# Kernel optimization log

Measured on AMD Instinct MI355X. Metric: run time of the kernel, lower is better.

## Reference

```python
import jax, jax.numpy as jnp
import numpy as np

N_NODES = 50000
N_EDGES = 800000
D = 64


def setup_inputs() -> dict:
    key = jax.random.key(0)
    k1, k2, k3, k4, k5 = jax.random.split(key, 5)
    x = jax.random.normal(k1, (N_NODES, D), dtype=jnp.float32)
    edge_index = jax.random.randint(k2, (2, N_EDGES), 0, N_NODES, dtype=jnp.int64)
    edge_weight = jax.random.uniform(k3, (N_EDGES,), dtype=jnp.float32)
    W = jax.random.normal(k4, (D, D), dtype=jnp.float32) / np.sqrt(D)
    b = jax.random.normal(k5, (D,), dtype=jnp.float32) * 0.01
    return {"x": x, "edge_index": edge_index, "edge_weight": edge_weight, "W": W, "b": b}


def reference(x, edge_index, edge_weight, W, b):
    # GCNConv (PyG defaults): add self-loops (weight 1), symmetric normalization,
    # linear transform then normalized scatter-add aggregation, bias, then ReLU.
    n = x.shape[0]
    loop = jnp.arange(n, dtype=edge_index.dtype)
    src = jnp.concatenate([edge_index[0], loop])          # [E+N] message sources
    dst = jnp.concatenate([edge_index[1], loop])          # [E+N] message targets
    ew = jnp.concatenate([edge_weight, jnp.ones((n,), dtype=x.dtype)])
    # degree on target nodes from edge weights
    deg = jax.ops.segment_sum(ew, dst, num_segments=n)
    dinv = jnp.where(deg > 0, jax.lax.rsqrt(deg), 0.0)
    norm = dinv[src] * ew * dinv[dst]                      # [E+N]
    h = x @ W                                              # [N, D] linear first
    msg = h[src] * norm[:, None]                           # gather + scale
    out = jax.ops.segment_sum(msg, dst, num_segments=n) + b
    return jax.nn.relu(out)
```

## Files before the change

kernel.cpp:

```cpp
#include <hip/hip_runtime.h>

#define N_NODES 50000
#define N_EDGES 800000
#define D 64
#define NBUCK 782
#define BINBLK 256
#define EPB 3125
#define ECHUNK 13
#define GEMMBLK ((N_NODES + 15) / 16)
#define CAP 1536
#define FIXSCALE 4194304.0f


__device__ inline unsigned short f2bf(float f) {
    unsigned u = __float_as_uint(f);
    unsigned r = (u + 0x7FFFu + ((u >> 16) & 1u)) >> 16;
    return (unsigned short)r;
}
__device__ inline float bf2f(unsigned short h) {
    return __uint_as_float(((unsigned)h) << 16);
}
__device__ inline int wave_incl_scan(int v, int lane) {
#pragma unroll
    for (int off = 1; off < 64; off <<= 1) {
        int n = __shfl_up(v, off, 64);
        if (lane >= off) v += n;
    }
    return v;
}


__global__ void k_zero(int* __restrict__ gcur) {
    int i = blockIdx.x * blockDim.x + threadIdx.x;
    if (i < NBUCK) gcur[i] = 0;
}

union ShU {
    int lh[NBUCK];
    struct { float Ws[D][D]; float Xs[4][D]; } gm;
};
__global__ __launch_bounds__(256) void k_bin_gemm(
        const int* __restrict__ src, const int* __restrict__ dst,
        const float* __restrict__ ew,
        int* __restrict__ gcur, unsigned long long* __restrict__ binned,
        const float* __restrict__ x, const float* __restrict__ W,
        unsigned short* __restrict__ hb) {
    __shared__ ShU sh;
    int t = threadIdx.x;
    if (blockIdx.x < BINBLK) {
        int rd[ECHUNK]; int rs[ECHUNK]; float rw[ECHUNK];
        int* lh = sh.lh;
        for (int i = t; i < NBUCK; i += 256) lh[i] = 0;
        __syncthreads();
        int base = blockIdx.x * EPB;
#pragma unroll
        for (int i = 0; i < ECHUNK; ++i) {
            int k = i * 256 + t;
            rd[i] = -1;
            if (k < EPB) {
                int e = base + k;
                rd[i] = dst[e];
                rs[i] = src[e];
                rw[i] = ew[e];
                atomicAdd(&lh[rd[i] >> 6], 1);
            }
        }
        __syncthreads();
        for (int i = t; i < NBUCK; i += 256) {
            int c = lh[i];
            lh[i] = (c > 0) ? atomicAdd(&gcur[i], c) : 0;
        }
        __syncthreads();
#pragma unroll
        for (int i = 0; i < ECHUNK; ++i) {
            if (rd[i] >= 0) {
                int bkt = rd[i] >> 6;
                int pos = atomicAdd(&lh[bkt], 1);
                if (pos < CAP)
                    binned[(size_t)bkt * CAP + pos] =
                        ((unsigned long long)__float_as_uint(rw[i]) << 32)
                      | ((unsigned)rs[i] << 16) | (unsigned)rd[i];
            }
        }
    } else {
        float (*Ws)[D] = sh.gm.Ws;
        float (*Xs)[D] = sh.gm.Xs;
        for (int k = t; k < D * D; k += 256) Ws[k / D][k % D] = W[k];
        int base = (blockIdx.x - BINBLK) * 16;
        int r = t >> 6, c = t & 63;
        for (int g = 0; g < 4; ++g) {
            int row = base + g * 4 + r;
            __syncthreads();
            Xs[r][c] = (row < N_NODES) ? x[(size_t)row * D + c] : 0.0f;
            __syncthreads();
            float acc = 0.0f;
#pragma unroll
            for (int k = 0; k < D; ++k) acc = fmaf(Xs[r][k], Ws[k][c], acc);
            if (row < N_NODES) hb[(size_t)row * D + c] = f2bf(acc);
        }
    }
}

__global__ void k_sortbucket(const unsigned long long* __restrict__ binned,
                             const int* __restrict__ gcur,
                             unsigned* __restrict__ csr,
                             unsigned* __restrict__ rc,
                             float* __restrict__ dinv) {
    __shared__ unsigned long long stage[CAP];
    __shared__ unsigned long long cw[64];
    __shared__ int off2[64];
    int t = threadIdx.x;
    if (t < 64) cw[t] = 0ULL;
    __syncthreads();
    int b = blockIdx.x;
    size_t beg = (size_t)b * CAP;
    int len = min(gcur[b], CAP);
    for (int k = t; k < len; k += 256) {
        unsigned long long p = binned[beg + k];
        stage[k] = p;
        int dl = (int)(p & 63);
        float w = __uint_as_float((unsigned)(p >> 32));
        atomicAdd(&cw[dl], (1ULL << 40) | (unsigned long long)__float2uint_rn(w * FIXSCALE));
    }
    __syncthreads();
    if (t < 64) {
        int c = (int)(cw[t] >> 40);
        float wfix = (float)(cw[t] & ((1ULL << 40) - 1ULL));
        int inc = wave_incl_scan(c, t);
        int excl = inc - c;
        off2[t] = excl;
        int node = b * 64 + t;
        if (node < N_NODES) {
            rc[node] = ((unsigned)c << 12) | (unsigned)excl;
            dinv[node] = rsqrtf(1.0f + wfix * (1.0f / FIXSCALE));
        }
    }
    __syncthreads();
    for (int k = t; k < len; k += 256) {
        unsigned long long p = stage[k];
        int dl = (int)(p & 63);
        int r = atomicAdd(&off2[dl], 1);
        unsigned short ewb = f2bf(__uint_as_float((unsigned)(p >> 32)));
        csr[beg + r] = ((unsigned)ewb << 16) | (unsigned)((p >> 16) & 0xffffu);
    }
}

__global__ void k_aggregate(const unsigned short* __restrict__ hb,
                            const float* __restrict__ dinv,
                            const unsigned* __restrict__ rc,
                            const unsigned* __restrict__ csr,
                            const float* __restrict__ bias,
                            float* __restrict__ out) {
    int node = blockIdx.x * 4 + (threadIdx.x >> 6);
    int lane = threadIdx.x & 63;
    if (node >= N_NODES) return;
    int half = lane >> 5;
    int cl = lane & 31;
    float di = dinv[node];
    unsigned r = rc[node];
    int cnt = (int)(r >> 12);
    size_t beg = (size_t)(node >> 6) * CAP + (r & 0xFFFu);
    float a0 = 0.0f, a1 = 0.0f, p0 = 0.0f, p1 = 0.0f;
    {
        unsigned hd = *(const unsigned*)(hb + (size_t)node * D + 2 * cl);
        float m = (half == 0) ? di : 0.0f;
        a0 = m * bf2f((unsigned short)hd);
        a1 = m * bf2f((unsigned short)(hd >> 16));
    }
    for (int b0 = 0; b0 < cnt; b0 += 64) {
        int n = min(64, cnt - b0);
        int my_src = 0;
        float my_ew = 0.0f;
        if (lane < n) {
            unsigned q = csr[beg + b0 + lane];
            my_src = (int)(q & 0xffffu);
            my_ew = bf2f((unsigned short)(q >> 16)) * dinv[my_src];
        }
        int jp = 0;
        for (; jp + 3 < n; jp += 4) {
            int iA = jp + half, iB = jp + 2 + half;
            int sA = __shfl(my_src, iA, 64);
            float eA = __shfl(my_ew, iA, 64);
            int sB = __shfl(my_src, iB, 64);
            float eB = __shfl(my_ew, iB, 64);
            unsigned hA = *(const unsigned*)(hb + (size_t)sA * D + 2 * cl);
            unsigned hB = *(const unsigned*)(hb + (size_t)sB * D + 2 * cl);
            a0 = fmaf(bf2f((unsigned short)hA), eA, a0);
            a1 = fmaf(bf2f((unsigned short)(hA >> 16)), eA, a1);
            p0 = fmaf(bf2f((unsigned short)hB), eB, p0);
            p1 = fmaf(bf2f((unsigned short)(hB >> 16)), eB, p1);
        }
        for (; jp + 1 < n; jp += 2) {
            int iA = jp + half;
            int sA = __shfl(my_src, iA, 64);
            float eA = __shfl(my_ew, iA, 64);
            unsigned hA = *(const unsigned*)(hb + (size_t)sA * D + 2 * cl);
            a0 = fmaf(bf2f((unsigned short)hA), eA, a0);
            a1 = fmaf(bf2f((unsigned short)(hA >> 16)), eA, a1);
        }
        if (jp < n) {
            int sA = __shfl(my_src, jp, 64);
            float eA = __shfl(my_ew, jp, 64);
            unsigned hA = *(const unsigned*)(hb + (size_t)sA * D + 2 * cl);
            float m = (half == 0) ? eA : 0.0f;
            a0 = fmaf(bf2f((unsigned short)hA), m, a0);
            a1 = fmaf(bf2f((unsigned short)(hA >> 16)), m, a1);
        }
    }
    a0 += p0; a1 += p1;
    a0 += __shfl_xor(a0, 32, 64);
    a1 += __shfl_xor(a1, 32, 64);
    if (half == 0) {
        float v0 = fmaf(di, a0, bias[2 * cl]);
        float v1 = fmaf(di, a1, bias[2 * cl + 1]);
        float2 o;
        o.x = fmaxf(v0, 0.0f);
        o.y = fmaxf(v1, 0.0f);
        *(float2*)(out + (size_t)node * D + 2 * cl) = o;
    }
}


extern "C" void kernel_launch(void* const* d_in, const int* in_sizes, int n_in,
                              void* d_out, int out_size, void* d_ws, size_t ws_size,
                              hipStream_t stream) {
    const float* x  = (const float*)d_in[0];
    const int*   ei = (const int*)d_in[1];
    const float* ew = (const float*)d_in[2];
    const float* W  = (const float*)d_in[3];
    const float* b  = (const float*)d_in[4];
    float* out = (float*)d_out;

    const int* src = ei;
    const int* dst = ei + N_EDGES;

    unsigned long long* binned = (unsigned long long*)d_ws;
    unsigned* csr      = (unsigned*)(binned + (size_t)NBUCK * CAP);
    int*   gcur        = (int*)(csr + (size_t)NBUCK * CAP);
    unsigned* rc       = (unsigned*)(gcur + 1024);
    float* dinv        = (float*)(rc + 50048);
    unsigned short* hb = (unsigned short*)(dinv + 50048);

    dim3 blk(256);
    k_zero<<<4, blk, 0, stream>>>(gcur);
    k_bin_gemm<<<BINBLK + GEMMBLK, blk, 0, stream>>>(src, dst, ew, gcur, binned,
                                                     x, W, hb);
    k_sortbucket<<<NBUCK, blk, 0, stream>>>(binned, gcur, csr, rc, dinv);
    k_aggregate<<<(N_NODES + 3) / 4, blk, 0, stream>>>(hb, dinv, rc, csr, b, out);
}
```

Before: 76.01 us.

## Widen aggregate gathers to 16-byte loads, pad bucket counters, use memset

The aggregation kernel now has each lane load 8 bf16 features (uint4) instead of 2, with 8 edges handled per wave step, which cuts the number of load instructions and shuffles per edge. Its reduction uses three xor shuffles and float4 stores. Bucket counters are spaced 16 ints apart to reduce atomic contention and false sharing between neighbouring counters. The zeroing kernel is replaced by hipMemsetAsync. The cost is more registers per lane and masked work on partial 16-edge tails, which may waste lanes for nodes with low degree.

New measurement: 78.28 us. 3.0% more time.

```diff
diff --git a/kernel.cpp b/kernel.cpp
--- a/kernel.cpp
+++ b/kernel.cpp
@@ -9,6 +9,7 @@
 #define ECHUNK 13
 #define GEMMBLK ((N_NODES + 15) / 16)
 #define CAP 1536
+#define GSTRIDE 16
 #define FIXSCALE 4194304.0f
 
 
@@ -29,11 +30,6 @@
     return v;
 }
 
-
-__global__ void k_zero(int* __restrict__ gcur) {
-    int i = blockIdx.x * blockDim.x + threadIdx.x;
-    if (i < NBUCK) gcur[i] = 0;
-}
 
 union ShU {
     int lh[NBUCK];
@@ -68,7 +64,7 @@
         __syncthreads();
         for (int i = t; i < NBUCK; i += 256) {
             int c = lh[i];
-            lh[i] = (c > 0) ? atomicAdd(&gcur[i], c) : 0;
+            lh[i] = (c > 0) ? atomicAdd(&gcur[(size_t)i * GSTRIDE], c) : 0;
         }
         __syncthreads();
 #pragma unroll
@@ -114,7 +110,7 @@
     __syncthreads();
     int b = blockIdx.x;
     size_t beg = (size_t)b * CAP;
-    int len = min(gcur[b], CAP);
+    int len = min(gcur[(size_t)b * GSTRIDE], CAP);
     for (int k = t; k < len; k += 256) {
         unsigned long long p = binned[beg + k];
         stage[k] = p;
@@ -154,19 +150,27 @@
     int node = blockIdx.x * 4 + (threadIdx.x >> 6);
     int lane = threadIdx.x & 63;
     if (node >= N_NODES) return;
-    int half = lane >> 5;
-    int cl = lane & 31;
+    int oct = lane >> 3;
+    int c8 = lane & 7;
     float di = dinv[node];
     unsigned r = rc[node];
     int cnt = (int)(r >> 12);
     size_t beg = (size_t)(node >> 6) * CAP + (r & 0xFFFu);
-    float a0 = 0.0f, a1 = 0.0f, p0 = 0.0f, p1 = 0.0f;
+    float a[8], p[8];
     {
-        unsigned hd = *(const unsigned*)(hb + (size_t)node * D + 2 * cl);
-        float m = (half == 0) ? di : 0.0f;
-        a0 = m * bf2f((unsigned short)hd);
-        a1 = m * bf2f((unsigned short)(hd >> 16));
-    }
+        uint4 hd = *(const uint4*)(hb + (size_t)node * D + 8 * c8);
+        float m = (oct == 0) ? di : 0.0f;
+        a[0] = m * bf2f((unsigned short)hd.x);
+        a[1] = m * bf2f((unsigned short)(hd.x >> 16));
+        a[2] = m * bf2f((unsigned short)hd.y);
+        a[3] = m * bf2f((unsigned short)(hd.y >> 16));
+        a[4] = m * bf2f((unsigned short)hd.z);
+        a[5] = m * bf2f((unsigned short)(hd.z >> 16));
+        a[6] = m * bf2f((unsigned short)hd.w);
+        a[7] = m * bf2f((unsigned short)(hd.w >> 16));
+    }
+#pragma unroll
+    for (int i = 0; i < 8; ++i) p[i] = 0.0f;
     for (int b0 = 0; b0 < cnt; b0 += 64) {
         int n = min(64, cnt - b0);
         int my_src = 0;
@@ -177,46 +181,78 @@
             my_ew = bf2f((unsigned short)(q >> 16)) * dinv[my_src];
         }
         int jp = 0;
-        for (; jp + 3 < n; jp += 4) {
-            int iA = jp + half, iB = jp + 2 + half;
+        for (; jp + 16 <= n; jp += 16) {
+            int iA = jp + oct, iB = iA + 8;
             int sA = __shfl(my_src, iA, 64);
             float eA = __shfl(my_ew, iA, 64);
             int sB = __shfl(my_src, iB, 64);
             float eB = __shfl(my_ew, iB, 64);
-            unsigned hA = *(const unsigned*)(hb + (size_t)sA * D + 2 * cl);
-            unsigned hB = *(const unsigned*)(hb + (size_t)sB * D + 2 * cl);
-            a0 = fmaf(bf2f((unsigned short)hA), eA, a0);
-            a1 = fmaf(bf2f((unsigned short)(hA >> 16)), eA, a1);
-            p0 = fmaf(bf2f((unsigned short)hB), eB, p0);
-            p1 = fmaf(bf2f((unsigned short)(hB >> 16)), eB, p1);
-        }
-        for (; jp + 1 < n; jp += 2) {
-            int iA = jp + half;
+            uint4 hA = *(const uint4*)(hb + (size_t)sA * D + 8 * c8);
+            uint4 hB = *(const uint4*)(hb + (size_t)sB * D + 8 * c8);
+            a[0] = fmaf(bf2f((unsigned short)hA.x), eA, a[0]);
+            a[1] = fmaf(bf2f((unsigned short)(hA.x >> 16)), eA, a[1]);
+            a[2] = fmaf(bf2f((unsigned short)hA.y), eA, a[2]);
+            a[3] = fmaf(bf2f((unsigned short)(hA.y >> 16)), eA, a[3]);
+            a[4] = fmaf(bf2f((unsigned short)hA.z), eA, a[4]);
+            a[5] = fmaf(bf2f((unsigned short)(hA.z >> 16)), eA, a[5]);
+            a[6] = fmaf(bf2f((unsigned short)hA.w), eA, a[6]);
+            a[7] = fmaf(bf2f((unsigned short)(hA.w >> 16)), eA, a[7]);
+            p[0] = fmaf(bf2f((unsigned short)hB.x), eB, p[0]);
+            p[1] = fmaf(bf2f((unsigned short)(hB.x >> 16)), eB, p[1]);
+            p[2] = fmaf(bf2f((unsigned short)hB.y), eB, p[2]);
+            p[3] = fmaf(bf2f((unsigned short)(hB.y >> 16)), eB, p[3]);
+            p[4] = fmaf(bf2f((unsigned short)hB.z), eB, p[4]);
+            p[5] = fmaf(bf2f((unsigned short)(hB.z >> 16)), eB, p[5]);
+            p[6] = fmaf(bf2f((unsigned short)hB.w), eB, p[6]);
+            p[7] = fmaf(bf2f((unsigned short)(hB.w >> 16)), eB, p[7]);
+        }
+        if (jp < n) {
+            int iA = jp + oct, iB = iA + 8;
             int sA = __shfl(my_src, iA, 64);
             float eA = __shfl(my_ew, iA, 64);
-            unsigned hA = *(const unsigned*)(hb + (size_t)sA * D + 2 * cl);
-            a0 = fmaf(bf2f((unsigned short)hA), eA, a0);
-            a1 = fmaf(bf2f((unsigned short)(hA >> 16)), eA, a1);
-        }
-        if (jp < n) {
-            int sA = __shfl(my_src, jp, 64);
-            float eA = __shfl(my_ew, jp, 64);
-            unsigned hA = *(const unsigned*)(hb + (size_t)sA * D + 2 * cl);
-            float m = (half == 0) ? eA : 0.0f;
-            a0 = fmaf(bf2f((unsigned short)hA), m, a0);
-            a1 = fmaf(bf2f((unsigned short)(hA >> 16)), m, a1);
-        }
-    }
-    a0 += p0; a1 += p1;
-    a0 += __shfl_xor(a0, 32, 64);
-    a1 += __shfl_xor(a1, 32, 64);
-    if (half == 0) {
-        float v0 = fmaf(di, a0, bias[2 * cl]);
-        float v1 = fmaf(di, a1, bias[2 * cl + 1]);
-        float2 o;
-        o.x = fmaxf(v0, 0.0f);
-        o.y = fmaxf(v1, 0.0f);
-        *(float2*)(out + (size_t)node * D + 2 * cl) = o;
+            int sB = __shfl(my_src, iB, 64);
+            float eB = __shfl(my_ew, iB, 64);
+            eA = (iA < n) ? eA : 0.0f;
+            eB = (iB < n) ? eB : 0.0f;
+            uint4 hA = *(const uint4*)(hb + (size_t)sA * D + 8 * c8);
+            uint4 hB = *(const uint4*)(hb + (size_t)sB * D + 8 * c8);
+            a[0] = fmaf(bf2f((unsigned short)hA.x), eA, a[0]);
+            a[1] = fmaf(bf2f((unsigned short)(hA.x >> 16)), eA, a[1]);
+            a[2] = fmaf(bf2f((unsigned short)hA.y), eA, a[2]);
+            a[3] = fmaf(bf2f((unsigned short)(hA.y >> 16)), eA, a[3]);
+            a[4] = fmaf(bf2f((unsigned short)hA.z), eA, a[4]);
+            a[5] = fmaf(bf2f((unsigned short)(hA.z >> 16)), eA, a[5]);
+            a[6] = fmaf(bf2f((unsigned short)hA.w), eA, a[6]);
+            a[7] = fmaf(bf2f((unsigned short)(hA.w >> 16)), eA, a[7]);
+            p[0] = fmaf(bf2f((unsigned short)hB.x), eB, p[0]);
+            p[1] = fmaf(bf2f((unsigned short)(hB.x >> 16)), eB, p[1]);
+            p[2] = fmaf(bf2f((unsigned short)hB.y), eB, p[2]);
+            p[3] = fmaf(bf2f((unsigned short)(hB.y >> 16)), eB, p[3]);
+            p[4] = fmaf(bf2f((unsigned short)hB.z), eB, p[4]);
+            p[5] = fmaf(bf2f((unsigned short)(hB.z >> 16)), eB, p[5]);
+            p[6] = fmaf(bf2f((unsigned short)hB.w), eB, p[6]);
+            p[7] = fmaf(bf2f((unsigned short)(hB.w >> 16)), eB, p[7]);
+        }
+    }
+#pragma unroll
+    for (int i = 0; i < 8; ++i) {
+        a[i] += p[i];
+        a[i] += __shfl_xor(a[i], 8, 64);
+        a[i] += __shfl_xor(a[i], 16, 64);
+        a[i] += __shfl_xor(a[i], 32, 64);
+    }
+    if (oct == 0) {
+        float4 o0, o1;
+        o0.x = fmaxf(fmaf(di, a[0], bias[8 * c8 + 0]), 0.0f);
+        o0.y = fmaxf(fmaf(di, a[1], bias[8 * c8 + 1]), 0.0f);
+        o0.z = fmaxf(fmaf(di, a[2], bias[8 * c8 + 2]), 0.0f);
+        o0.w = fmaxf(fmaf(di, a[3], bias[8 * c8 + 3]), 0.0f);
+        o1.x = fmaxf(fmaf(di, a[4], bias[8 * c8 + 4]), 0.0f);
+        o1.y = fmaxf(fmaf(di, a[5], bias[8 * c8 + 5]), 0.0f);
+        o1.z = fmaxf(fmaf(di, a[6], bias[8 * c8 + 6]), 0.0f);
+        o1.w = fmaxf(fmaf(di, a[7], bias[8 * c8 + 7]), 0.0f);
+        *(float4*)(out + (size_t)node * D + 8 * c8) = o0;
+        *(float4*)(out + (size_t)node * D + 8 * c8 + 4) = o1;
     }
 }
 
@@ -237,12 +273,12 @@
     unsigned long long* binned = (unsigned long long*)d_ws;
     unsigned* csr      = (unsigned*)(binned + (size_t)NBUCK * CAP);
     int*   gcur        = (int*)(csr + (size_t)NBUCK * CAP);
-    unsigned* rc       = (unsigned*)(gcur + 1024);
+    unsigned* rc       = (unsigned*)(gcur + NBUCK * GSTRIDE + 16);
     float* dinv        = (float*)(rc + 50048);
     unsigned short* hb = (unsigned short*)(dinv + 50048);
 
     dim3 blk(256);
-    k_zero<<<4, blk, 0, stream>>>(gcur);
+    (void)hipMemsetAsync(gcur, 0, (size_t)NBUCK * GSTRIDE * sizeof(int), stream);
     k_bin_gemm<<<BINBLK + GEMMBLK, blk, 0, stream>>>(src, dst, ew, gcur, binned,
                                                      x, W, hb);
     k_sortbucket<<<NBUCK, blk, 0, stream>>>(binned, gcur, csr, rc, dinv);
```
